# Optimization experiments

Hardware: AMD Instinct MI355X
Metric: run time of the kernel (lower is better)

## Reference

```python
import jax, jax.numpy as jnp
import numpy as np

T, N, D = 4, 4096, 64      # tasks, nodes, inp_dim
E = 2                      # edge_dim
OUT = 64                   # out_dim
H0 = 2 * OUT               # first conv layer width (n_layer=2 -> 2*out_dim)
EPS = 1e-12                # F.normalize p=1 eps
SLOPE = 0.01               # LeakyReLU default negative_slope


def setup_inputs() -> dict:
    key = jax.random.key(0)
    k1, k2, k3, k4 = jax.random.split(key, 4)
    node_feat = jax.random.normal(k1, (T, N, D), dtype=jnp.float32)
    edge_feat = jax.random.uniform(k2, (T, E, N, N), dtype=jnp.float32)
    cin = (E + 1) * D  # conv0 in_channels
    # 1x1 conv kernels stored as [out, in] matrices (kernel_size=1, bias=False)
    w0 = jax.random.normal(k3, (H0, cin), dtype=jnp.float32) * (1.0 / np.sqrt(cin))
    w1 = jax.random.normal(k4, (OUT, H0), dtype=jnp.float32) * (1.0 / np.sqrt(H0))
    return {"node_feat": node_feat, "edge_feat": edge_feat, "w0": w0, "w1": w1}


def reference(node_feat, edge_feat, w0, w1):
    t, n, d = node_feat.shape
    e = edge_feat.shape[1]
    # zero the diagonal (no self-edges), then L1-normalize each row
    diag_mask = 1.0 - jnp.eye(n, dtype=node_feat.dtype)  # [N, N], broadcasts over T,E
    masked = edge_feat * diag_mask
    denom = jnp.maximum(jnp.sum(jnp.abs(masked), axis=-1, keepdims=True), EPS)
    norm_edge = masked / denom  # [T, E, N, N]
    # aggregate neighbor features per edge channel: [T, E, N, D]
    aggr = jnp.einsum('tenm,tmd->tend', norm_edge, node_feat)
    # concat [node_feat, aggr_e0, aggr_e1, ...] along feature dim -> [T, N, (E+1)*D]
    aggr_flat = aggr.transpose(0, 2, 1, 3).reshape(t, n, e * d)
    x = jnp.concatenate([node_feat, aggr_flat], axis=-1)
    # 1x1-conv MLP == per-node linear layers with LeakyReLU
    h = jax.nn.leaky_relu(jnp.einsum('tnc,hc->tnh', x, w0), SLOPE)
    out = jax.nn.leaky_relu(jnp.einsum('tnh,oh->tno', h, w1), SLOPE)
    return out  # [T, N, OUT]
```

## Files before the change

### kernel.cpp

```cpp
#include <hip/hip_runtime.h>
#include <hip/hip_bf16.h>
#include <stdint.h>

#define T_   4
#define E_   2
#define NN   4096
#define H0_  128
#define OUT_ 64
#define CIN_ 192

using short8   = __attribute__((ext_vector_type(8))) short;
using ushort8  = __attribute__((ext_vector_type(8))) unsigned short;
using ushort4v = __attribute__((ext_vector_type(4))) unsigned short;
using f32x4    = __attribute__((ext_vector_type(4))) float;

__device__ __forceinline__ uint16_t f2bf(float f) {
  union { __hip_bfloat16 h; uint16_t u; } v;
  v.h = __float2bfloat16(f);
  return v.u;
}
__device__ __forceinline__ float bf2f(uint16_t b) {
  return __uint_as_float(((uint32_t)b) << 16);
}
__device__ __forceinline__ ushort4v cvt4v(const f32x4& v) {
  ushort4v r;
  r[0] = f2bf(v[0]); r[1] = f2bf(v[1]); r[2] = f2bf(v[2]); r[3] = f2bf(v[3]);
  return r;
}

#define A_IDX(r, k) (((r) << 6) + ((k) ^ (((r) & 7) << 3)))
#define B_IDX(c, k) (((c) << 6) + ((k) ^ (((c) & 7) << 3)))

#define MFMA(A, B, C) C = __builtin_amdgcn_mfma_f32_16x16x32_bf16(A, B, C, 0, 0, 0)

#define BT_ELEMS (T_ * 80 * NN)
#define W0_ELEMS (H0_ * CIN_)
#define W1_ELEMS (OUT_ * H0_)

__global__ void pack_kernel(const float* __restrict__ node,
                            const float* __restrict__ w0,
                            const float* __restrict__ w1,
                            uint16_t* __restrict__ Bt,
                            float* __restrict__ w0t,
                            float* __restrict__ w1t) {
  int idx = blockIdx.x * 256 + threadIdx.x;
  if (idx < BT_ELEMS) {
    int m  = idx & (NN - 1);
    int tc = idx >> 12;
    int t  = tc / 80;
    int c  = tc - t * 80;
    uint16_t v;
    if (c < 64)       v = f2bf(node[(((size_t)(t << 12) + m) << 6) + c]);
    else if (c == 64) v = 0x3f80;
    else              v = 0;
    Bt[idx] = v;
  } else if (idx < BT_ELEMS + W0_ELEMS) {
    int i = idx - BT_ELEMS;
    int j = i & 127, k = i >> 7;
    w0t[i] = w0[j * CIN_ + k];
  } else if (idx < BT_ELEMS + W0_ELEMS + W1_ELEMS) {
    int i = idx - BT_ELEMS - W0_ELEMS;
    int j = i & 63, k = i >> 6;
    w1t[i] = w1[j * H0_ + k];
  }
}

__global__ __launch_bounds__(256, 2)
void aggr_kernel(const float* __restrict__ edge,
                 const float* __restrict__ node,
                 const uint16_t* __restrict__ Bt,
                 float* __restrict__ aggr) {
  __shared__ uint16_t As[2][64 * 64];
  __shared__ uint16_t Bs[2][80 * 64];
  __shared__ float den_lds[4][16];

  const int tid  = threadIdx.x;
  const int lane = tid & 63;
  const int w    = tid >> 6;
  const int te   = blockIdx.y;
  const int t    = te >> 1;
  const int rowbase = blockIdx.x * 64;
  const int phase = (blockIdx.x * 5 + blockIdx.y * 8) & 63;

  const float*    Ag = edge + (size_t)te * NN * NN + (size_t)rowbase * NN;
  const uint16_t* Bg = Bt + (size_t)t * 80 * NN;

  const int arow = tid >> 4;
  const int akg  = (tid & 15) << 2;
  const int bcol = tid >> 3;
  const int bk8  = (tid & 7) << 3;

  f32x4 acc0 = {0,0,0,0}, acc1 = {0,0,0,0}, acc2 = {0,0,0,0},
        acc3 = {0,0,0,0}, acc4 = {0,0,0,0};

  f32x4   as0_A, as1_A, as2_A, as3_A, as0_B, as1_B, as2_B, as3_B;
  ushort8 bs0_A, bs1_A, bs0_B, bs1_B;

#define STAGE_LOAD(KT, S)                                                     \
  { const int ktp = ((KT) + phase) & 63;                                      \
    const float* ap = Ag + (size_t)ktp * 64 + akg;                            \
    as0##S = __builtin_nontemporal_load((const f32x4*)(ap + (size_t)(arow      ) * NN)); \
    as1##S = __builtin_nontemporal_load((const f32x4*)(ap + (size_t)(arow + 16) * NN)); \
    as2##S = __builtin_nontemporal_load((const f32x4*)(ap + (size_t)(arow + 32) * NN)); \
    as3##S = __builtin_nontemporal_load((const f32x4*)(ap + (size_t)(arow + 48) * NN)); \
    const uint16_t* bp = Bg + (size_t)ktp * 64 + bk8;                         \
    bs0##S = *(const ushort8*)(bp + (size_t)(bcol      ) * NN);               \
    bs1##S = *(const ushort8*)(bp + (size_t)(bcol + 32) * NN); }

#define STAGE_WRITE(S, BUF)                                                   \
  { *(ushort4v*)&As[BUF][A_IDX(arow,      akg)] = cvt4v(as0##S);              \
    *(ushort4v*)&As[BUF][A_IDX(arow + 16, akg)] = cvt4v(as1##S);              \
    *(ushort4v*)&As[BUF][A_IDX(arow + 32, akg)] = cvt4v(as2##S);              \
    *(ushort4v*)&As[BUF][A_IDX(arow + 48, akg)] = cvt4v(as3##S);              \
    *(ushort8*)&Bs[BUF][B_IDX(bcol,      bk8)] = bs0##S;                      \
    *(ushort8*)&Bs[BUF][B_IDX(bcol + 32, bk8)] = bs1##S; }

#define COMPUTE(BUF)                                                          \
  { const int ar = (w << 4) + (lane & 15);                                    \
    const int kk = (lane >> 4) << 3;                                          \
    const int cb = lane & 15;                                                 \
    const uint16_t* Ab = &As[BUF][0];                                         \
    const uint16_t* Bb = &Bs[BUF][0];                                         \
    short8 a0 = *(const short8*)(Ab + A_IDX(ar, kk));                         \
    short8 a1 = *(const short8*)(Ab + A_IDX(ar, kk + 32));                    \
    short8 b;                                                                 \
    b = *(const short8*)(Bb + B_IDX(cb,      kk));      MFMA(a0, b, acc0);    \
    b = *(const short8*)(Bb + B_IDX(cb,      kk + 32)); MFMA(a1, b, acc0);    \
    b = *(const short8*)(Bb + B_IDX(cb + 16, kk));      MFMA(a0, b, acc1);    \
    b = *(const short8*)(Bb + B_IDX(cb + 16, kk + 32)); MFMA(a1, b, acc1);    \
    b = *(const short8*)(Bb + B_IDX(cb + 32, kk));      MFMA(a0, b, acc2);    \
    b = *(const short8*)(Bb + B_IDX(cb + 32, kk + 32)); MFMA(a1, b, acc2);    \
    b = *(const short8*)(Bb + B_IDX(cb + 48, kk));      MFMA(a0, b, acc3);    \
    b = *(const short8*)(Bb + B_IDX(cb + 48, kk + 32)); MFMA(a1, b, acc3);    \
    b = *(const short8*)(Bb + B_IDX(cb + 64, kk));      MFMA(a0, b, acc4);    \
    b = *(const short8*)(Bb + B_IDX(cb + 64, kk + 32)); MFMA(a1, b, acc4); }

  if (tid < 128) {
    int col = 64 + (tid >> 3);
    int k8  = (tid & 7) << 3;
    ushort8 v = {0, 0, 0, 0, 0, 0, 0, 0};
    if (col == 64) {
      ushort8 o = {0x3f80, 0x3f80, 0x3f80, 0x3f80, 0x3f80, 0x3f80, 0x3f80, 0x3f80};
      v = o;
    }
    *(ushort8*)&Bs[0][B_IDX(col, k8)] = v;
    *(ushort8*)&Bs[1][B_IDX(col, k8)] = v;
  }

  STAGE_LOAD(0, _A);
  STAGE_LOAD(1, _B);
  STAGE_WRITE(_A, 0);
  __syncthreads();

  int cur = 0;
  for (int kt = 0; kt < 64; kt += 2) {
    if (kt < 62) STAGE_LOAD(kt + 2, _A);
    COMPUTE(cur);
    STAGE_WRITE(_B, cur ^ 1);
    __syncthreads();
    cur ^= 1;
    if (kt < 61) STAGE_LOAD(kt + 3, _B);
    COMPUTE(cur);
    if (kt < 62) {
      STAGE_WRITE(_A, cur ^ 1);
      __syncthreads();
      cur ^= 1;
    }
  }

  if ((lane & 15) == 0) {
    int rq = (lane >> 4) << 2;
    den_lds[w][rq + 0] = acc4[0];
    den_lds[w][rq + 1] = acc4[1];
    den_lds[w][rq + 2] = acc4[2];
    den_lds[w][rq + 3] = acc4[3];
  }
  __syncthreads();

  {
    const int q  = lane >> 4;
    const int c0 = lane & 15;
    const float* nodeT = node + ((size_t)t * NN << 6);
#pragma unroll
    for (int i = 0; i < 4; ++i) {
      int m    = (q << 2) + i;
      int grow = rowbase + (w << 4) + m;
      float dv  = bf2f(f2bf(edge[(size_t)te * NN * NN + (size_t)grow * NN + grow]));
      float den = den_lds[w][m] - dv;
      float inv = 1.0f / fmaxf(den, 1e-12f);
      const float* nr = nodeT + ((size_t)grow << 6);
      float v0 = (acc0[i] - dv * bf2f(f2bf(nr[c0 +  0]))) * inv;
      float v1 = (acc1[i] - dv * bf2f(f2bf(nr[c0 + 16]))) * inv;
      float v2 = (acc2[i] - dv * bf2f(f2bf(nr[c0 + 32]))) * inv;
      float v3 = (acc3[i] - dv * bf2f(f2bf(nr[c0 + 48]))) * inv;
      float* op = aggr + (((size_t)te * NN + grow) << 6) + c0;
      __builtin_nontemporal_store(v0, op);
      __builtin_nontemporal_store(v1, op + 16);
      __builtin_nontemporal_store(v2, op + 32);
      __builtin_nontemporal_store(v3, op + 48);
    }
  }
#undef STAGE_LOAD
#undef STAGE_WRITE
#undef COMPUTE
}

__global__ __launch_bounds__(256)
void mlp_kernel(const float* __restrict__ node,
                const float* __restrict__ aggr,
                const float* __restrict__ w0t,
                const float* __restrict__ w1t,
                float* __restrict__ out) {
  __shared__ float h_lds[16][128];

  const int tid = threadIdx.x;
  const int j   = tid & 63;
  const int w   = tid >> 6;
  const int g0  = blockIdx.x * 16 + w * 4;
  const int t   = g0 >> 12;
  const int n0  = g0 & (NN - 1);

  const float* x0 = node + (((size_t)t * NN + n0) << 6);
  const float* x1 = aggr + (((size_t)(t * 2 + 0) * NN + n0) << 6);
  const float* x2 = aggr + (((size_t)(t * 2 + 1) * NN + n0) << 6);

  float h0[4] = {0, 0, 0, 0};
  float h1[4] = {0, 0, 0, 0};

#pragma unroll
  for (int s = 0; s < 3; ++s) {
    const float* xs = (s == 0) ? x0 : (s == 1) ? x1 : x2;
#pragma unroll
    for (int k4 = 0; k4 < 16; ++k4) {
      int kk = s * 64 + k4 * 4;
      float wa0 = w0t[(kk + 0) * 128 + j];
      float wa1 = w0t[(kk + 1) * 128 + j];
      float wa2 = w0t[(kk + 2) * 128 + j];
      float wa3 = w0t[(kk + 3) * 128 + j];
      float wb0 = w0t[(kk + 0) * 128 + 64 + j];
      float wb1 = w0t[(kk + 1) * 128 + 64 + j];
      float wb2 = w0t[(kk + 2) * 128 + 64 + j];
      float wb3 = w0t[(kk + 3) * 128 + 64 + j];
#pragma unroll
      for (int q = 0; q < 4; ++q) {
        float4 xv = *(const float4*)(xs + (q << 6) + k4 * 4);
        h0[q] += xv.x * wa0 + xv.y * wa1 + xv.z * wa2 + xv.w * wa3;
        h1[q] += xv.x * wb0 + xv.y * wb1 + xv.z * wb2 + xv.w * wb3;
      }
    }
  }
#pragma unroll
  for (int q = 0; q < 4; ++q) {
    float a = h0[q]; a = (a > 0.0f) ? a : 0.01f * a;
    float b = h1[q]; b = (b > 0.0f) ? b : 0.01f * b;
    h_lds[w * 4 + q][j]      = a;
    h_lds[w * 4 + q][64 + j] = b;
  }
  __syncthreads();

  float o[4] = {0, 0, 0, 0};
#pragma unroll
  for (int k4 = 0; k4 < 32; ++k4) {
    float w10 = w1t[(k4 * 4 + 0) * 64 + j];
    float w11 = w1t[(k4 * 4 + 1) * 64 + j];
    float w12 = w1t[(k4 * 4 + 2) * 64 + j];
    float w13 = w1t[(k4 * 4 + 3) * 64 + j];
#pragma unroll
    for (int q = 0; q < 4; ++q) {
      float4 hv = *(const float4*)&h_lds[w * 4 + q][k4 * 4];
      o[q] += hv.x * w10 + hv.y * w11 + hv.z * w12 + hv.w * w13;
    }
  }
#pragma unroll
  for (int q = 0; q < 4; ++q) {
    float v = o[q]; v = (v > 0.0f) ? v : 0.01f * v;
    out[((size_t)(g0 + q) << 6) + j] = v;
  }
}

extern "C" void kernel_launch(void* const* d_in, const int* in_sizes, int n_in,
                              void* d_out, int out_size, void* d_ws, size_t ws_size,
                              hipStream_t stream) {
  const float* node = (const float*)d_in[0];
  const float* edge = (const float*)d_in[1];
  const float* w0   = (const float*)d_in[2];
  const float* w1   = (const float*)d_in[3];
  float* out = (float*)d_out;

  char* ws = (char*)d_ws;
  uint16_t* Bt   = (uint16_t*)ws;
  float*    aggr = (float*)(ws + 2621440);
  float*    w0t  = (float*)(ws + 2621440 + 8388608);
  float*    w1t  = (float*)(ws + 2621440 + 8388608 + 98304);

  pack_kernel<<<5248, 256, 0, stream>>>(node, w0, w1, Bt, w0t, w1t);

  dim3 g1(NN / 64, T_ * E_);
  aggr_kernel<<<g1, 256, 0, stream>>>(edge, node, Bt, aggr);

  mlp_kernel<<<(T_ * NN) / 16, 256, 0, stream>>>(node, aggr, w0t, w1t, out);
}
```

Before: 142.2 us.

## Batch edge-matrix loads into 256-column super-tiles with deeper prefetch

The aggregation kernel now issues all four 64-column A-tile loads of a 256-wide super-tile at once, so each thread reads 1 KB contiguous per row, and then drains them across four compute stages. The start-phase rotation moves to super-tile granularity. The aim is longer contiguous HBM bursts and more loads in flight to hide latency on the bandwidth-bound edge-matrix stream. The cost is many more live registers (16 f32x4 staging vectors), which could reduce occupancy under launch_bounds(256,2) or cause spills.

```diff
diff --git a/kernel.cpp b/kernel.cpp
--- a/kernel.cpp
+++ b/kernel.cpp
@@ -27,6 +27,7 @@
   r[0] = f2bf(v[0]); r[1] = f2bf(v[1]); r[2] = f2bf(v[2]); r[3] = f2bf(v[3]);
   return r;
 }
+#define NTL(p) __builtin_nontemporal_load((const f32x4*)(p))
 
 #define A_IDX(r, k) (((r) << 6) + ((k) ^ (((r) & 7) << 3)))
 #define B_IDX(c, k) (((c) << 6) + ((k) ^ (((c) & 7) << 3)))
@@ -79,8 +80,8 @@
   const int w    = tid >> 6;
   const int te   = blockIdx.y;
   const int t    = te >> 1;
-  const int rowbase = blockIdx.x * 64;
-  const int phase = (blockIdx.x * 5 + blockIdx.y * 8) & 63;
+  const int rowbase = blockIdx.x << 6;
+  const int phase16 = (blockIdx.x * 3 + blockIdx.y * 5) & 15;
 
   const float*    Ag = edge + (size_t)te * NN * NN + (size_t)rowbase * NN;
   const uint16_t* Bg = Bt + (size_t)t * 80 * NN;
@@ -90,29 +91,39 @@
   const int bcol = tid >> 3;
   const int bk8  = (tid & 7) << 3;
 
+#define PHKT(KT) ((((((KT) >> 2) + phase16) & 15) << 2) | ((KT) & 3))
+
   f32x4 acc0 = {0,0,0,0}, acc1 = {0,0,0,0}, acc2 = {0,0,0,0},
         acc3 = {0,0,0,0}, acc4 = {0,0,0,0};
 
-  f32x4   as0_A, as1_A, as2_A, as3_A, as0_B, as1_B, as2_B, as3_B;
+  f32x4 aA00, aA01, aA02, aA03, aA10, aA11, aA12, aA13,
+        aA20, aA21, aA22, aA23, aA30, aA31, aA32, aA33;
   ushort8 bs0_A, bs1_A, bs0_B, bs1_B;
 
-#define STAGE_LOAD(KT, S)                                                     \
-  { const int ktp = ((KT) + phase) & 63;                                      \
-    const float* ap = Ag + (size_t)ktp * 64 + akg;                            \
-    as0##S = __builtin_nontemporal_load((const f32x4*)(ap + (size_t)(arow      ) * NN)); \
-    as1##S = __builtin_nontemporal_load((const f32x4*)(ap + (size_t)(arow + 16) * NN)); \
-    as2##S = __builtin_nontemporal_load((const f32x4*)(ap + (size_t)(arow + 32) * NN)); \
-    as3##S = __builtin_nontemporal_load((const f32x4*)(ap + (size_t)(arow + 48) * NN)); \
+#define LOADA_Q(SUP, Q)                                                       \
+  { const float* ap = Ag + (size_t)(((((SUP) + phase16) & 15) << 8) + ((Q) << 6) + akg); \
+    aA##Q##0 = NTL(ap + (size_t)(arow      ) * NN);                           \
+    aA##Q##1 = NTL(ap + (size_t)(arow + 16) * NN);                            \
+    aA##Q##2 = NTL(ap + (size_t)(arow + 32) * NN);                            \
+    aA##Q##3 = NTL(ap + (size_t)(arow + 48) * NN); }
+
+#define LOADSUPER(SUP) { LOADA_Q(SUP, 0); LOADA_Q(SUP, 1);                    \
+                         LOADA_Q(SUP, 2); LOADA_Q(SUP, 3); }
+
+#define WRITEA(Q, BUF)                                                        \
+  { *(ushort4v*)&As[BUF][A_IDX(arow,      akg)] = cvt4v(aA##Q##0);            \
+    *(ushort4v*)&As[BUF][A_IDX(arow + 16, akg)] = cvt4v(aA##Q##1);            \
+    *(ushort4v*)&As[BUF][A_IDX(arow + 32, akg)] = cvt4v(aA##Q##2);            \
+    *(ushort4v*)&As[BUF][A_IDX(arow + 48, akg)] = cvt4v(aA##Q##3); }
+
+#define LOADB(KT, S)                                                          \
+  { const int ktp = PHKT(KT);                                                 \
     const uint16_t* bp = Bg + (size_t)ktp * 64 + bk8;                         \
     bs0##S = *(const ushort8*)(bp + (size_t)(bcol      ) * NN);               \
     bs1##S = *(const ushort8*)(bp + (size_t)(bcol + 32) * NN); }
 
-#define STAGE_WRITE(S, BUF)                                                   \
-  { *(ushort4v*)&As[BUF][A_IDX(arow,      akg)] = cvt4v(as0##S);              \
-    *(ushort4v*)&As[BUF][A_IDX(arow + 16, akg)] = cvt4v(as1##S);              \
-    *(ushort4v*)&As[BUF][A_IDX(arow + 32, akg)] = cvt4v(as2##S);              \
-    *(ushort4v*)&As[BUF][A_IDX(arow + 48, akg)] = cvt4v(as3##S);              \
-    *(ushort8*)&Bs[BUF][B_IDX(bcol,      bk8)] = bs0##S;                      \
+#define WRITEB(S, BUF)                                                        \
+  { *(ushort8*)&Bs[BUF][B_IDX(bcol,      bk8)] = bs0##S;                      \
     *(ushort8*)&Bs[BUF][B_IDX(bcol + 32, bk8)] = bs1##S; }
 
 #define COMPUTE(BUF)                                                          \
@@ -147,26 +158,48 @@
     *(ushort8*)&Bs[1][B_IDX(col, k8)] = v;
   }
 
-  STAGE_LOAD(0, _A);
-  STAGE_LOAD(1, _B);
-  STAGE_WRITE(_A, 0);
+  LOADSUPER(0);
+  LOADB(0, _A);
+  WRITEA(0, 0);
+  WRITEB(_A, 0);
   __syncthreads();
 
   int cur = 0;
-  for (int kt = 0; kt < 64; kt += 2) {
-    if (kt < 62) STAGE_LOAD(kt + 2, _A);
+  for (int kt4 = 0; kt4 < 64; kt4 += 4) {
+    const int sup = kt4 >> 2;
+    LOADB(kt4 + 1, _B);
     COMPUTE(cur);
-    STAGE_WRITE(_B, cur ^ 1);
-    __syncthreads();
-    cur ^= 1;
-    if (kt < 61) STAGE_LOAD(kt + 3, _B);
+    WRITEA(1, cur ^ 1);
+    WRITEB(_B, cur ^ 1);
+    __syncthreads(); cur ^= 1;
+    LOADB(kt4 + 2, _A);
     COMPUTE(cur);
-    if (kt < 62) {
-      STAGE_WRITE(_A, cur ^ 1);
-      __syncthreads();
-      cur ^= 1;
-    }
-  }
+    WRITEA(2, cur ^ 1);
+    WRITEB(_A, cur ^ 1);
+    __syncthreads(); cur ^= 1;
+    LOADB(kt4 + 3, _B);
+    COMPUTE(cur);
+    WRITEA(3, cur ^ 1);
+    WRITEB(_B, cur ^ 1);
+    __syncthreads(); cur ^= 1;
+    if (kt4 < 60) {
+      LOADSUPER(sup + 1);
+      LOADB(kt4 + 4, _A);
+      COMPUTE(cur);
+      WRITEA(0, cur ^ 1);
+      WRITEB(_A, cur ^ 1);
+      __syncthreads(); cur ^= 1;
+    } else {
+      COMPUTE(cur);
+    }
+  }
+#undef LOADA_Q
+#undef LOADSUPER
+#undef WRITEA
+#undef LOADB
+#undef WRITEB
+#undef COMPUTE
+#undef PHKT
 
   if ((lane & 15) == 0) {
     int rq = (lane >> 4) << 2;
@@ -200,9 +233,6 @@
       __builtin_nontemporal_store(v3, op + 48);
     }
   }
-#undef STAGE_LOAD
-#undef STAGE_WRITE
-#undef COMPUTE
 }
 
 __global__ __launch_bounds__(256)
```

New measurement: 153.1 us. 7.6% more time.

## Fuse MLP into aggregation kernel via last-arriver atomic counter

Applied to the files above, without the earlier changes.

Removes the separate MLP kernel launch. Each aggregation block writes its aggr tile, then increments a per-(task,row-tile) counter. The second of the two edge-channel blocks to finish runs the two-layer MLP for those 64 rows, reusing LDS for the hidden activations. This saves a launch and the gap between kernels, and lets the MLP overlap with other blocks' aggregation. In exchange it adds a fence and an atomic, the aggr stores are no longer nontemporal, and half the blocks carry a serial MLP tail with lower parallelism than the old separate grid.

```diff
diff --git a/kernel.cpp b/kernel.cpp
--- a/kernel.cpp
+++ b/kernel.cpp
@@ -27,6 +27,7 @@
   r[0] = f2bf(v[0]); r[1] = f2bf(v[1]); r[2] = f2bf(v[2]); r[3] = f2bf(v[3]);
   return r;
 }
+#define NTL(p) __builtin_nontemporal_load((const f32x4*)(p))
 
 #define A_IDX(r, k) (((r) << 6) + ((k) ^ (((r) & 7) << 3)))
 #define B_IDX(c, k) (((c) << 6) + ((k) ^ (((c) & 7) << 3)))
@@ -42,8 +43,10 @@
                             const float* __restrict__ w1,
                             uint16_t* __restrict__ Bt,
                             float* __restrict__ w0t,
-                            float* __restrict__ w1t) {
+                            float* __restrict__ w1t,
+                            int* __restrict__ cnt) {
   int idx = blockIdx.x * 256 + threadIdx.x;
+  if (idx < 256) cnt[idx] = 0;
   if (idx < BT_ELEMS) {
     int m  = idx & (NN - 1);
     int tc = idx >> 12;
@@ -69,10 +72,15 @@
 void aggr_kernel(const float* __restrict__ edge,
                  const float* __restrict__ node,
                  const uint16_t* __restrict__ Bt,
-                 float* __restrict__ aggr) {
+                 float* __restrict__ aggrWS,
+                 const float* __restrict__ w0t,
+                 const float* __restrict__ w1t,
+                 int* __restrict__ cnt,
+                 float* __restrict__ out) {
   __shared__ uint16_t As[2][64 * 64];
   __shared__ uint16_t Bs[2][80 * 64];
   __shared__ float den_lds[4][16];
+  __shared__ int second;
 
   const int tid  = threadIdx.x;
   const int lane = tid & 63;
@@ -99,10 +107,10 @@
 #define STAGE_LOAD(KT, S)                                                     \
   { const int ktp = ((KT) + phase) & 63;                                      \
     const float* ap = Ag + (size_t)ktp * 64 + akg;                            \
-    as0##S = __builtin_nontemporal_load((const f32x4*)(ap + (size_t)(arow      ) * NN)); \
-    as1##S = __builtin_nontemporal_load((const f32x4*)(ap + (size_t)(arow + 16) * NN)); \
-    as2##S = __builtin_nontemporal_load((const f32x4*)(ap + (size_t)(arow + 32) * NN)); \
-    as3##S = __builtin_nontemporal_load((const f32x4*)(ap + (size_t)(arow + 48) * NN)); \
+    as0##S = NTL(ap + (size_t)(arow      ) * NN);                             \
+    as1##S = NTL(ap + (size_t)(arow + 16) * NN);                              \
+    as2##S = NTL(ap + (size_t)(arow + 32) * NN);                              \
+    as3##S = NTL(ap + (size_t)(arow + 48) * NN);                              \
     const uint16_t* bp = Bg + (size_t)ktp * 64 + bk8;                         \
     bs0##S = *(const ushort8*)(bp + (size_t)(bcol      ) * NN);               \
     bs1##S = *(const ushort8*)(bp + (size_t)(bcol + 32) * NN); }
@@ -193,88 +201,90 @@
       float v1 = (acc1[i] - dv * bf2f(f2bf(nr[c0 + 16]))) * inv;
       float v2 = (acc2[i] - dv * bf2f(f2bf(nr[c0 + 32]))) * inv;
       float v3 = (acc3[i] - dv * bf2f(f2bf(nr[c0 + 48]))) * inv;
-      float* op = aggr + (((size_t)te * NN + grow) << 6) + c0;
-      __builtin_nontemporal_store(v0, op);
-      __builtin_nontemporal_store(v1, op + 16);
-      __builtin_nontemporal_store(v2, op + 32);
-      __builtin_nontemporal_store(v3, op + 48);
+      float* op = aggrWS + (((size_t)te * NN + grow) << 6) + c0;
+      op[0]  = v0;
+      op[16] = v1;
+      op[32] = v2;
+      op[48] = v3;
     }
   }
 #undef STAGE_LOAD
 #undef STAGE_WRITE
 #undef COMPUTE
-}
-
-__global__ __launch_bounds__(256)
-void mlp_kernel(const float* __restrict__ node,
-                const float* __restrict__ aggr,
-                const float* __restrict__ w0t,
-                const float* __restrict__ w1t,
-                float* __restrict__ out) {
-  __shared__ float h_lds[16][128];
-
-  const int tid = threadIdx.x;
-  const int j   = tid & 63;
-  const int w   = tid >> 6;
-  const int g0  = blockIdx.x * 16 + w * 4;
-  const int t   = g0 >> 12;
-  const int n0  = g0 & (NN - 1);
-
-  const float* x0 = node + (((size_t)t * NN + n0) << 6);
-  const float* x1 = aggr + (((size_t)(t * 2 + 0) * NN + n0) << 6);
-  const float* x2 = aggr + (((size_t)(t * 2 + 1) * NN + n0) << 6);
-
-  float h0[4] = {0, 0, 0, 0};
-  float h1[4] = {0, 0, 0, 0};
-
-#pragma unroll
-  for (int s = 0; s < 3; ++s) {
-    const float* xs = (s == 0) ? x0 : (s == 1) ? x1 : x2;
-#pragma unroll
-    for (int k4 = 0; k4 < 16; ++k4) {
-      int kk = s * 64 + k4 * 4;
-      float wa0 = w0t[(kk + 0) * 128 + j];
-      float wa1 = w0t[(kk + 1) * 128 + j];
-      float wa2 = w0t[(kk + 2) * 128 + j];
-      float wa3 = w0t[(kk + 3) * 128 + j];
-      float wb0 = w0t[(kk + 0) * 128 + 64 + j];
-      float wb1 = w0t[(kk + 1) * 128 + 64 + j];
-      float wb2 = w0t[(kk + 2) * 128 + 64 + j];
-      float wb3 = w0t[(kk + 3) * 128 + 64 + j];
+
+  __threadfence();
+  __syncthreads();
+  if (tid == 0) {
+    second = atomicAdd(&cnt[t * 64 + blockIdx.x], 1);
+  }
+  __syncthreads();
+  if (second == 0) return;
+  __threadfence();
+
+  {
+    float* hshare = (float*)&As[0][0];
+    const int j = lane;
+    const float* x0b = node   + (((size_t)t * NN + rowbase) << 6);
+    const float* x1b = aggrWS + (((size_t)(t * 2 + 0) * NN + rowbase) << 6);
+    const float* x2b = aggrWS + (((size_t)(t * 2 + 1) * NN + rowbase) << 6);
+    float* outb = out + (((size_t)t * NN + rowbase) << 6);
+
+    for (int g4 = 0; g4 < 4; ++g4) {
+      const int r0 = (w << 4) + (g4 << 2);
+      const float* x0 = x0b + ((size_t)r0 << 6);
+      const float* x1 = x1b + ((size_t)r0 << 6);
+      const float* x2 = x2b + ((size_t)r0 << 6);
+
+      float h0[4] = {0, 0, 0, 0};
+      float h1[4] = {0, 0, 0, 0};
+#pragma unroll
+      for (int s = 0; s < 3; ++s) {
+        const float* xs = (s == 0) ? x0 : (s == 1) ? x1 : x2;
+#pragma unroll
+        for (int k4 = 0; k4 < 16; ++k4) {
+          int kk = s * 64 + k4 * 4;
+          float wa0 = w0t[(kk + 0) * 128 + j];
+          float wa1 = w0t[(kk + 1) * 128 + j];
+          float wa2 = w0t[(kk + 2) * 128 + j];
+          float wa3 = w0t[(kk + 3) * 128 + j];
+          float wb0 = w0t[(kk + 0) * 128 + 64 + j];
+          float wb1 = w0t[(kk + 1) * 128 + 64 + j];
+          float wb2 = w0t[(kk + 2) * 128 + 64 + j];
+          float wb3 = w0t[(kk + 3) * 128 + 64 + j];
+#pragma unroll
+          for (int q = 0; q < 4; ++q) {
+            float4 xv = *(const float4*)(xs + (q << 6) + k4 * 4);
+            h0[q] += xv.x * wa0 + xv.y * wa1 + xv.z * wa2 + xv.w * wa3;
+            h1[q] += xv.x * wb0 + xv.y * wb1 + xv.z * wb2 + xv.w * wb3;
+          }
+        }
+      }
 #pragma unroll
       for (int q = 0; q < 4; ++q) {
-        float4 xv = *(const float4*)(xs + (q << 6) + k4 * 4);
-        h0[q] += xv.x * wa0 + xv.y * wa1 + xv.z * wa2 + xv.w * wa3;
-        h1[q] += xv.x * wb0 + xv.y * wb1 + xv.z * wb2 + xv.w * wb3;
+        float a = h0[q]; a = (a > 0.0f) ? a : 0.01f * a;
+        float b = h1[q]; b = (b > 0.0f) ? b : 0.01f * b;
+        hshare[(w * 4 + q) * 128 + j]      = a;
+        hshare[(w * 4 + q) * 128 + 64 + j] = b;
+      }
+      float o[4] = {0, 0, 0, 0};
+#pragma unroll
+      for (int k4 = 0; k4 < 32; ++k4) {
+        float w10 = w1t[(k4 * 4 + 0) * 64 + j];
+        float w11 = w1t[(k4 * 4 + 1) * 64 + j];
+        float w12 = w1t[(k4 * 4 + 2) * 64 + j];
+        float w13 = w1t[(k4 * 4 + 3) * 64 + j];
+#pragma unroll
+        for (int q = 0; q < 4; ++q) {
+          float4 hv = *(const float4*)(hshare + (w * 4 + q) * 128 + k4 * 4);
+          o[q] += hv.x * w10 + hv.y * w11 + hv.z * w12 + hv.w * w13;
+        }
+      }
+#pragma unroll
+      for (int q = 0; q < 4; ++q) {
+        float v = o[q]; v = (v > 0.0f) ? v : 0.01f * v;
+        outb[((size_t)(r0 + q) << 6) + j] = v;
       }
     }
-  }
-#pragma unroll
-  for (int q = 0; q < 4; ++q) {
-    float a = h0[q]; a = (a > 0.0f) ? a : 0.01f * a;
-    float b = h1[q]; b = (b > 0.0f) ? b : 0.01f * b;
-    h_lds[w * 4 + q][j]      = a;
-    h_lds[w * 4 + q][64 + j] = b;
-  }
-  __syncthreads();
-
-  float o[4] = {0, 0, 0, 0};
-#pragma unroll
-  for (int k4 = 0; k4 < 32; ++k4) {
-    float w10 = w1t[(k4 * 4 + 0) * 64 + j];
-    float w11 = w1t[(k4 * 4 + 1) * 64 + j];
-    float w12 = w1t[(k4 * 4 + 2) * 64 + j];
-    float w13 = w1t[(k4 * 4 + 3) * 64 + j];
-#pragma unroll
-    for (int q = 0; q < 4; ++q) {
-      float4 hv = *(const float4*)&h_lds[w * 4 + q][k4 * 4];
-      o[q] += hv.x * w10 + hv.y * w11 + hv.z * w12 + hv.w * w13;
-    }
-  }
-#pragma unroll
-  for (int q = 0; q < 4; ++q) {
-    float v = o[q]; v = (v > 0.0f) ? v : 0.01f * v;
-    out[((size_t)(g0 + q) << 6) + j] = v;
   }
 }
 
@@ -292,11 +302,10 @@
   float*    aggr = (float*)(ws + 2621440);
   float*    w0t  = (float*)(ws + 2621440 + 8388608);
   float*    w1t  = (float*)(ws + 2621440 + 8388608 + 98304);
-
-  pack_kernel<<<5248, 256, 0, stream>>>(node, w0, w1, Bt, w0t, w1t);
+  int*      cnt  = (int*)(ws + 2621440 + 8388608 + 98304 + 32768);
+
+  pack_kernel<<<5248, 256, 0, stream>>>(node, w0, w1, Bt, w0t, w1t, cnt);
 
   dim3 g1(NN / 64, T_ * E_);
-  aggr_kernel<<<g1, 256, 0, stream>>>(edge, node, Bt, aggr);
-
-  mlp_kernel<<<(T_ * NN) / 16, 256, 0, stream>>>(node, aggr, w0t, w1t, out);
-}
+  aggr_kernel<<<g1, 256, 0, stream>>>(edge, node, Bt, aggr, w0t, w1t, cnt, out);
+}
```

New measurement: 506.3 us. 3.56x slower.
